# Optimization experiments

Hardware: AMD Instinct MI355X
Metric: run time of the kernel (lower is better)

The kernel has to match this reference:

```python
import jax, jax.numpy as jnp
import numpy as np

BETA = 0.95      # LIF membrane decay (init arg)
THR = 1.0        # snntorch Leaky default threshold
NUM_STEPS = 128


@jax.custom_vjp
def spike(x):
    # Heaviside fire with ATan surrogate gradient (snntorch default, alpha=2)
    return (x > 0).astype(x.dtype)

def _spike_fwd(x):
    return spike(x), x

def _spike_bwd(x, g):
    return (g / (1.0 + (jnp.pi * x) ** 2),)

spike.defvjp(_spike_fwd, _spike_bwd)


def setup_inputs() -> dict:
    key = jax.random.key(0)
    ks = jax.random.split(key, 5)
    B, NI, NH, NO = 2048, 1024, 2048, 10
    return {
        "x": jax.random.normal(ks[0], (B, NI), dtype=jnp.float32),
        "w1": jax.random.normal(ks[1], (NH, NI), dtype=jnp.float32) * 0.05,
        "b1": jax.random.normal(ks[2], (NH,), dtype=jnp.float32) * 0.05,
        "w2": jax.random.normal(ks[3], (NO, NH), dtype=jnp.float32) * 0.05,
        "b2": jax.random.normal(ks[4], (NO,), dtype=jnp.float32) * 0.05,
    }


def reference(x, w1, b1, w2, b2):
    # fc1(x) is loop-invariant: compute the input current once.
    cur1 = jnp.einsum("bi,hi->bh", x, w1) + b1  # [B, NH]
    mem1_0 = jnp.zeros_like(cur1)
    mem2_0 = jnp.zeros((x.shape[0], w2.shape[0]), dtype=x.dtype)

    def step(carry, _):
        mem1, mem2 = carry
        # snntorch Leaky, reset-by-subtraction; reset term is detached.
        reset1 = jax.lax.stop_gradient((mem1 > THR).astype(mem1.dtype))
        mem1 = BETA * mem1 + cur1 - reset1 * THR
        spk1 = spike(mem1 - THR)
        cur2 = jnp.einsum("bh,oh->bo", spk1, w2) + b2  # [B, NO]
        reset2 = jax.lax.stop_gradient((mem2 > THR).astype(mem2.dtype))
        mem2 = BETA * mem2 + cur2 - reset2 * THR
        spk2 = spike(mem2 - THR)
        return (mem1, mem2), (spk2, mem2)

    _, (spk2_rec, mem2_rec) = jax.lax.scan(step, (mem1_0, mem2_0), None, length=NUM_STEPS)
    return spk2_rec, mem2_rec  # each [T, B, NO]
```

## Files before the change

kernel.cpp:

```cpp
#include <hip/hip_runtime.h>
#include <hip/hip_bf16.h>


#define B_   2048
#define NI_  1024
#define NH_  2048
#define NO_  10
#define T_   128

typedef __attribute__((ext_vector_type(8))) short short8;
typedef __attribute__((ext_vector_type(4))) float f32x4;
typedef __attribute__((ext_vector_type(4))) unsigned int u32x4;

__device__ __forceinline__ unsigned int bf16_rne(float f) {
  unsigned int u = __float_as_uint(f);
  return (u + 0x7FFFu + ((u >> 16) & 1u)) >> 16;
}

#define G_ASTRIDE 144
#define G_AOFF    0
#define G_BOFF    (128 * G_ASTRIDE)
#define G_SMEM    (2 * 128 * G_ASTRIDE)

__global__ __launch_bounds__(512, 2) void gemm_cur1(
    const float* __restrict__ x, const float* __restrict__ w1,
    const float* __restrict__ b1, float* __restrict__ cur1) {
  __shared__ __align__(16) char smem[G_SMEM];
  const int tid = threadIdx.x;
  const int lane = tid & 63;
  const int wv = tid >> 6;
  const int wm = wv >> 2;
  const int wn = wv & 3;
  const int n15 = lane & 15;
  const int g = lane >> 4;
  const int brow = blockIdx.y * 128;
  const int bcol = blockIdx.x * 128;
  const int r_st = tid >> 3;
  const int kq = tid & 7;

  f32x4 acc[4][2];
#pragma unroll
  for (int tm = 0; tm < 4; ++tm)
#pragma unroll
    for (int tn = 0; tn < 2; ++tn) acc[tm][tn] = f32x4{0, 0, 0, 0};

  for (int kt = 0; kt < NI_; kt += 32) {
#pragma unroll
    for (int p = 0; p < 2; ++p) {
      const int r = r_st + p * 64;
      const float4 va = *reinterpret_cast<const float4*>(
          &x[(size_t)(brow + r) * NI_ + kt + kq * 4]);
      const float4 vb = *reinterpret_cast<const float4*>(
          &w1[(size_t)(bcol + r) * NI_ + kt + kq * 4]);
      const float fa[4] = {va.x, va.y, va.z, va.w};
      const float fb[4] = {vb.x, vb.y, vb.z, vb.w};
      unsigned ha[4], la[4], hb[4], lb[4];
#pragma unroll
      for (int c = 0; c < 4; ++c) {
        ha[c] = bf16_rne(fa[c]);
        la[c] = bf16_rne(fa[c] - __uint_as_float(ha[c] << 16));
        hb[c] = bf16_rne(fb[c]);
        lb[c] = bf16_rne(fb[c] - __uint_as_float(hb[c] << 16));
      }
      char* arow = smem + G_AOFF + r * G_ASTRIDE;
      char* brw  = smem + G_BOFF + r * G_ASTRIDE;
      *reinterpret_cast<uint2*>(arow + kq * 8) =
          uint2{ha[0] | (ha[1] << 16), ha[2] | (ha[3] << 16)};
      *reinterpret_cast<uint2*>(arow + 64 + kq * 8) =
          uint2{la[0] | (la[1] << 16), la[2] | (la[3] << 16)};
      *reinterpret_cast<uint2*>(brw + kq * 8) =
          uint2{hb[0] | (hb[1] << 16), hb[2] | (hb[3] << 16)};
      *reinterpret_cast<uint2*>(brw + 64 + kq * 8) =
          uint2{lb[0] | (lb[1] << 16), lb[2] | (lb[3] << 16)};
    }
    __syncthreads();

    short8 bh2[2], bl2[2];
#pragma unroll
    for (int tn = 0; tn < 2; ++tn) {
      const char* p = smem + G_BOFF + (wn * 32 + tn * 16 + n15) * G_ASTRIDE;
      bh2[tn] = *reinterpret_cast<const short8*>(p + g * 16);
      bl2[tn] = *reinterpret_cast<const short8*>(p + 64 + g * 16);
    }
#pragma unroll
    for (int tm = 0; tm < 4; ++tm) {
      const char* p = smem + G_AOFF + (wm * 64 + tm * 16 + n15) * G_ASTRIDE;
      const short8 ah = *reinterpret_cast<const short8*>(p + g * 16);
      const short8 al = *reinterpret_cast<const short8*>(p + 64 + g * 16);
#pragma unroll
      for (int tn = 0; tn < 2; ++tn) {
        acc[tm][tn] = __builtin_amdgcn_mfma_f32_16x16x32_bf16(
            ah, bh2[tn], acc[tm][tn], 0, 0, 0);
        acc[tm][tn] = __builtin_amdgcn_mfma_f32_16x16x32_bf16(
            ah, bl2[tn], acc[tm][tn], 0, 0, 0);
        acc[tm][tn] = __builtin_amdgcn_mfma_f32_16x16x32_bf16(
            al, bh2[tn], acc[tm][tn], 0, 0, 0);
      }
    }
    __syncthreads();
  }

#pragma unroll
  for (int tn = 0; tn < 2; ++tn) {
    const int col = bcol + wn * 32 + tn * 16 + n15;
    const float bias = b1[col];
#pragma unroll
    for (int tm = 0; tm < 4; ++tm) {
      const int rowb = brow + wm * 64 + tm * 16 + g * 4;
#pragma unroll
      for (int r = 0; r < 4; ++r)
        cur1[(size_t)(rowb + r) * NH_ + col] = acc[tm][tn][r] + bias;
    }
  }
}

__global__ __launch_bounds__(512, 4) void spikegen(
    const float* __restrict__ cur1, unsigned char* __restrict__ bits8) {
  const int lane = threadIdx.x & 63;
  const int w = threadIdx.x >> 6;
  const int bq = w >> 2;
  const int qf = w & 3;
  const int bb = blockIdx.x * 2 + bq;

  float mem1[8], c1v[8], c1m[8], cc[8];
  {
    const float* base = cur1 + (size_t)bb * NH_ + qf * 512 + lane * 8;
#pragma unroll
    for (int q = 0; q < 2; ++q) {
      const float4 v = *reinterpret_cast<const float4*>(base + q * 4);
      c1v[q * 4 + 0] = v.x; c1v[q * 4 + 1] = v.y;
      c1v[q * 4 + 2] = v.z; c1v[q * 4 + 3] = v.w;
    }
#pragma unroll
    for (int i = 0; i < 8; ++i) {
      mem1[i] = 0.0f;
      c1m[i] = c1v[i] - 1.0f;
      cc[i] = c1v[i];
    }
  }

  const float vone = 1.0f;
  unsigned char* dst = bits8 + (size_t)bb * T_ * 256 + qf * 64 + lane;
  for (int t = 0; t < T_; ++t) {
    float Wf = 0.0f;
#pragma unroll
    for (int i = 7; i >= 0; --i) {
      const float m = fmaf(0.95f, mem1[i], cc[i]);
      mem1[i] = m;
      const bool c = m > 1.0f;
      const float s = c ? vone : 0.0f;
      Wf = fmaf(2.0f, Wf, s);
      cc[i] = c ? c1m[i] : c1v[i];
    }
    dst[t * 256] = (unsigned char)(unsigned)Wf;
  }
}

#define SO_TC 16

__global__ __launch_bounds__(512, 2) void snn_out(
    const unsigned* __restrict__ bitsg, const float* __restrict__ w2,
    const float* __restrict__ b2, float* __restrict__ spk2_rec,
    float* __restrict__ mem2_rec) {
  __shared__ uint2 lut[16];
  __shared__ __align__(16) unsigned bitsl[64 * 68];
  __shared__ __align__(16) float comb[8 * 640];
  const int tid = threadIdx.x;
  const int lane = tid & 63;
  const int w = tid >> 6;
  const int bbase = blockIdx.x * 4;

  if (tid < 16) {
    lut[tid] = uint2{(tid & 1 ? 0x3F80u : 0u) | (tid & 2 ? 0x3F800000u : 0u),
                     (tid & 4 ? 0x3F80u : 0u) | (tid & 8 ? 0x3F800000u : 0u)};
  }

  u32x4 bhi[8];
  {
    const int o = lane & 15;
    const int koff = (lane >> 4) * 8;
#pragma unroll
    for (int kbl = 0; kbl < 8; ++kbl) {
      const int kb = w * 8 + kbl;
      unsigned int hw[4];
#pragma unroll
      for (int p = 0; p < 4; ++p) {
        unsigned int h0 = 0, h1 = 0;
        if (o < NO_) {
          const int k = kb * 32 + koff + p * 2;
          h0 = bf16_rne(w2[(size_t)o * NH_ + k]);
          h1 = bf16_rne(w2[(size_t)o * NH_ + k + 1]);
        }
        hw[p] = h0 | (h1 << 16);
      }
      bhi[kbl] = u32x4{hw[0], hw[1], hw[2], hw[3]};
    }
  }

  float mem2 = 0.0f, spk2 = 0.0f, b2v = 0.0f;
  float *srec = nullptr, *mrec = nullptr;
  if (w < 4 && lane < NO_) {
    b2v = b2[lane];
    srec = spk2_rec + (size_t)(bbase + w) * NO_ + lane;
    mrec = mem2_rec + (size_t)(bbase + w) * NO_ + lane;
  }

  const int n15 = lane & 15;
  const int g = lane >> 4;
  const unsigned char* bytes = reinterpret_cast<const unsigned char*>(bitsl);

  for (int ch = 0; ch < T_ / SO_TC; ++ch) {
#pragma unroll
    for (int j = 0; j < 2; ++j) {
      const int q = tid + j * 512;
      const int row = q >> 4;
      const int kq = q & 15;
      const int b = row >> 4, tl = row & 15;
      const uint4 v = *reinterpret_cast<const uint4*>(
          bitsg + ((size_t)(bbase + b) * T_ + ch * SO_TC + tl) * 64 + kq * 4);
      *reinterpret_cast<uint4*>(bitsl + row * 68 + kq * 4) = v;
    }
    __syncthreads();

#pragma unroll
    for (int b = 0; b < 4; ++b) {
      const int rbase = ((b * SO_TC + n15) * 68 + w * 8) * 4 + g;
      f32x4 acc = {0.0f, 0.0f, 0.0f, 0.0f};
#pragma unroll
      for (int kbl = 0; kbl < 8; ++kbl) {
        const unsigned byt = bytes[rbase + kbl * 4];
        const uint2 lo2 = lut[byt & 15u];
        const uint2 hi2 = lut[byt >> 4];
        const u32x4 A = {lo2.x, lo2.y, hi2.x, hi2.y};
        const short8 af = __builtin_bit_cast(short8, A);
        acc = __builtin_amdgcn_mfma_f32_16x16x32_bf16(
            af, __builtin_bit_cast(short8, bhi[kbl]), acc, 0, 0, 0);
      }
      if (n15 < NO_)
        *reinterpret_cast<f32x4*>(
            &comb[w * 640 + b * 160 + g * 40 + n15 * 4]) = acc;
    }
    __syncthreads();

    if (w < 4 && lane < NO_) {
      const float* cbase = comb + w * 160 + lane * 4;
#pragma unroll
      for (int tl = 0; tl < SO_TC; ++tl) {
        const int off = (tl >> 2) * 40 + (tl & 3);
        float s = 0.0f;
#pragma unroll
        for (int kk = 0; kk < 8; ++kk) s += cbase[kk * 640 + off];
        const float cur2 = s + b2v;
        float m = fmaf(0.95f, mem2, cur2);
        m = m - spk2;
        mem2 = m;
        spk2 = (m > 1.0f) ? 1.0f : 0.0f;
        const int t = ch * SO_TC + tl;
        srec[(size_t)t * (B_ * NO_)] = spk2;
        mrec[(size_t)t * (B_ * NO_)] = m;
      }
    }
  }
}

#define CUR1_BYTES ((size_t)B_ * NH_ * 4)
#define BITS_BYTES ((size_t)B_ * T_ * 64 * 4)

extern "C" void kernel_launch(void* const* d_in, const int* in_sizes, int n_in,
                              void* d_out, int out_size, void* d_ws, size_t ws_size,
                              hipStream_t stream) {
  const float* x  = (const float*)d_in[0];
  const float* w1 = (const float*)d_in[1];
  const float* b1 = (const float*)d_in[2];
  const float* w2 = (const float*)d_in[3];
  const float* b2 = (const float*)d_in[4];
  float* out = (float*)d_out;
  float* cur1 = (float*)d_ws;
  unsigned* bitsg = (unsigned*)((char*)d_ws + CUR1_BYTES);

  float* spk2_rec = out;
  float* mem2_rec = out + (size_t)T_ * B_ * NO_;

  dim3 g1(NH_ / 128, B_ / 128);
  gemm_cur1<<<g1, 512, 0, stream>>>(x, w1, b1, cur1);
  spikegen<<<B_ / 2, 512, 0, stream>>>(cur1, (unsigned char*)bitsg);
  snn_out<<<B_ / 4, 512, 0, stream>>>(bitsg, w2, b2, spk2_rec, mem2_rec);
}
```

Before: 170.8 us.

## Precompute split-bf16 operands in a separate pass and run GEMM over concatenated K

Adds a conversion kernel that splits x and w1 into bf16 hi/lo parts once and lays them out as a 3072-wide K dimension (hi,hi,lo for x and hi,lo,hi for w1), so the three-product split-precision GEMM becomes a plain bf16 GEMM. The GEMM no longer repeats the float-to-bf16 conversion inside every tile, which removes redundant conversion work, and its tile shrinks to 64x128 so more blocks are launched. The cost is an extra kernel launch plus writing and re-reading roughly 37 MB of converted operands. The converted buffers sit in workspace memory that the spike-bits buffer also uses, which is safe only because the GEMM finishes before spikegen writes there.

```diff
diff --git a/kernel.cpp b/kernel.cpp
--- a/kernel.cpp
+++ b/kernel.cpp
@@ -7,6 +7,7 @@
 #define NH_  2048
 #define NO_  10
 #define T_   128
+#define KP   3072
 
 typedef __attribute__((ext_vector_type(8))) short short8;
 typedef __attribute__((ext_vector_type(4))) float f32x4;
@@ -17,15 +18,45 @@
   return (u + 0x7FFFu + ((u >> 16) & 1u)) >> 16;
 }
 
-#define G_ASTRIDE 144
-#define G_AOFF    0
-#define G_BOFF    (128 * G_ASTRIDE)
-#define G_SMEM    (2 * 128 * G_ASTRIDE)
+__global__ __launch_bounds__(256) void convert_hl(
+    const float* __restrict__ x, const float* __restrict__ w1,
+    unsigned short* __restrict__ xc, unsigned short* __restrict__ w1c) {
+  const int gidx = blockIdx.x * 256 + threadIdx.x;
+  const int mat = gidx >> 19;
+  const int loc = gidx & 524287;
+  const int row = loc >> 8;
+  const int kq = loc & 255;
+
+  const float* src = (mat ? w1 : x) + (size_t)row * NI_ + kq * 4;
+  unsigned short* dst = (mat ? w1c : xc) + (size_t)row * KP + kq * 4;
+  const int hi2_off = mat ? 2048 : 1024;
+  const int lo_off  = mat ? 1024 : 2048;
+
+  const float4 v = *reinterpret_cast<const float4*>(src);
+  const float f[4] = {v.x, v.y, v.z, v.w};
+  unsigned h[4], l[4];
+#pragma unroll
+  for (int c = 0; c < 4; ++c) {
+    h[c] = bf16_rne(f[c]);
+    l[c] = bf16_rne(f[c] - __uint_as_float(h[c] << 16));
+  }
+  const uint2 hw = uint2{h[0] | (h[1] << 16), h[2] | (h[3] << 16)};
+  const uint2 lw = uint2{l[0] | (l[1] << 16), l[2] | (l[3] << 16)};
+  *reinterpret_cast<uint2*>(dst) = hw;
+  *reinterpret_cast<uint2*>(dst + hi2_off) = hw;
+  *reinterpret_cast<uint2*>(dst + lo_off) = lw;
+}
+
+#define RS 144
+#define GA_OFF 0
+#define GB_OFF (64 * RS)
+#define G2_SMEM (GB_OFF + 128 * RS)
 
 __global__ __launch_bounds__(512, 2) void gemm_cur1(
-    const float* __restrict__ x, const float* __restrict__ w1,
+    const unsigned short* __restrict__ xc,
+    const unsigned short* __restrict__ w1c,
     const float* __restrict__ b1, float* __restrict__ cur1) {
-  __shared__ __align__(16) char smem[G_SMEM];
+  __shared__ __align__(16) char smem[G2_SMEM];
   const int tid = threadIdx.x;
   const int lane = tid & 63;
   const int wv = tid >> 6;
@@ -33,69 +64,51 @@
   const int wn = wv & 3;
   const int n15 = lane & 15;
   const int g = lane >> 4;
-  const int brow = blockIdx.y * 128;
+  const int brow = blockIdx.y * 64;
   const int bcol = blockIdx.x * 128;
-  const int r_st = tid >> 3;
-  const int kq = tid & 7;
-
-  f32x4 acc[4][2];
-#pragma unroll
-  for (int tm = 0; tm < 4; ++tm)
+
+  const int s_row = tid >> 3;
+  const int s_o16 = tid & 7;
+
+  f32x4 acc[2][2];
+#pragma unroll
+  for (int tm = 0; tm < 2; ++tm)
 #pragma unroll
     for (int tn = 0; tn < 2; ++tn) acc[tm][tn] = f32x4{0, 0, 0, 0};
 
-  for (int kt = 0; kt < NI_; kt += 32) {
+  for (int kt = 0; kt < KP; kt += 64) {
+    {
+      const uint4 v = *reinterpret_cast<const uint4*>(
+          xc + (size_t)(brow + s_row) * KP + kt + s_o16 * 8);
+      *reinterpret_cast<uint4*>(smem + GA_OFF + s_row * RS + s_o16 * 16) = v;
+    }
 #pragma unroll
     for (int p = 0; p < 2; ++p) {
-      const int r = r_st + p * 64;
-      const float4 va = *reinterpret_cast<const float4*>(
-          &x[(size_t)(brow + r) * NI_ + kt + kq * 4]);
-      const float4 vb = *reinterpret_cast<const float4*>(
-          &w1[(size_t)(bcol + r) * NI_ + kt + kq * 4]);
-      const float fa[4] = {va.x, va.y, va.z, va.w};
-      const float fb[4] = {vb.x, vb.y, vb.z, vb.w};
-      unsigned ha[4], la[4], hb[4], lb[4];
-#pragma unroll
-      for (int c = 0; c < 4; ++c) {
-        ha[c] = bf16_rne(fa[c]);
-        la[c] = bf16_rne(fa[c] - __uint_as_float(ha[c] << 16));
-        hb[c] = bf16_rne(fb[c]);
-        lb[c] = bf16_rne(fb[c] - __uint_as_float(hb[c] << 16));
-      }
-      char* arow = smem + G_AOFF + r * G_ASTRIDE;
-      char* brw  = smem + G_BOFF + r * G_ASTRIDE;
-      *reinterpret_cast<uint2*>(arow + kq * 8) =
-          uint2{ha[0] | (ha[1] << 16), ha[2] | (ha[3] << 16)};
-      *reinterpret_cast<uint2*>(arow + 64 + kq * 8) =
-          uint2{la[0] | (la[1] << 16), la[2] | (la[3] << 16)};
-      *reinterpret_cast<uint2*>(brw + kq * 8) =
-          uint2{hb[0] | (hb[1] << 16), hb[2] | (hb[3] << 16)};
-      *reinterpret_cast<uint2*>(brw + 64 + kq * 8) =
-          uint2{lb[0] | (lb[1] << 16), lb[2] | (lb[3] << 16)};
+      const int s = tid + p * 512;
+      const int row = s >> 3, o16 = s & 7;
+      const uint4 v = *reinterpret_cast<const uint4*>(
+          w1c + (size_t)(bcol + row) * KP + kt + o16 * 8);
+      *reinterpret_cast<uint4*>(smem + GB_OFF + row * RS + o16 * 16) = v;
     }
     __syncthreads();
 
-    short8 bh2[2], bl2[2];
-#pragma unroll
-    for (int tn = 0; tn < 2; ++tn) {
-      const char* p = smem + G_BOFF + (wn * 32 + tn * 16 + n15) * G_ASTRIDE;
-      bh2[tn] = *reinterpret_cast<const short8*>(p + g * 16);
-      bl2[tn] = *reinterpret_cast<const short8*>(p + 64 + g * 16);
-    }
-#pragma unroll
-    for (int tm = 0; tm < 4; ++tm) {
-      const char* p = smem + G_AOFF + (wm * 64 + tm * 16 + n15) * G_ASTRIDE;
-      const short8 ah = *reinterpret_cast<const short8*>(p + g * 16);
-      const short8 al = *reinterpret_cast<const short8*>(p + 64 + g * 16);
-#pragma unroll
-      for (int tn = 0; tn < 2; ++tn) {
-        acc[tm][tn] = __builtin_amdgcn_mfma_f32_16x16x32_bf16(
-            ah, bh2[tn], acc[tm][tn], 0, 0, 0);
-        acc[tm][tn] = __builtin_amdgcn_mfma_f32_16x16x32_bf16(
-            ah, bl2[tn], acc[tm][tn], 0, 0, 0);
-        acc[tm][tn] = __builtin_amdgcn_mfma_f32_16x16x32_bf16(
-            al, bh2[tn], acc[tm][tn], 0, 0, 0);
-      }
+#pragma unroll
+    for (int kk = 0; kk < 2; ++kk) {
+      short8 af[2], bf[2];
+#pragma unroll
+      for (int tm = 0; tm < 2; ++tm)
+        af[tm] = *reinterpret_cast<const short8*>(
+            smem + GA_OFF + (wm * 32 + tm * 16 + n15) * RS + kk * 64 + g * 16);
+#pragma unroll
+      for (int tn = 0; tn < 2; ++tn)
+        bf[tn] = *reinterpret_cast<const short8*>(
+            smem + GB_OFF + (wn * 32 + tn * 16 + n15) * RS + kk * 64 + g * 16);
+#pragma unroll
+      for (int tm = 0; tm < 2; ++tm)
+#pragma unroll
+        for (int tn = 0; tn < 2; ++tn)
+          acc[tm][tn] = __builtin_amdgcn_mfma_f32_16x16x32_bf16(
+              af[tm], bf[tn], acc[tm][tn], 0, 0, 0);
     }
     __syncthreads();
   }
@@ -105,8 +118,8 @@
     const int col = bcol + wn * 32 + tn * 16 + n15;
     const float bias = b1[col];
 #pragma unroll
-    for (int tm = 0; tm < 4; ++tm) {
-      const int rowb = brow + wm * 64 + tm * 16 + g * 4;
+    for (int tm = 0; tm < 2; ++tm) {
+      const int rowb = brow + wm * 32 + tm * 16 + g * 4;
 #pragma unroll
       for (int r = 0; r < 4; ++r)
         cur1[(size_t)(rowb + r) * NH_ + col] = acc[tm][tn][r] + bias;
@@ -264,7 +277,6 @@
 }
 
 #define CUR1_BYTES ((size_t)B_ * NH_ * 4)
-#define BITS_BYTES ((size_t)B_ * T_ * 64 * 4)
 
 extern "C" void kernel_launch(void* const* d_in, const int* in_sizes, int n_in,
                               void* d_out, int out_size, void* d_ws, size_t ws_size,
@@ -276,13 +288,16 @@
   const float* b2 = (const float*)d_in[4];
   float* out = (float*)d_out;
   float* cur1 = (float*)d_ws;
+  unsigned short* xc  = (unsigned short*)((char*)d_ws + CUR1_BYTES);
+  unsigned short* w1c = xc + (size_t)2048 * KP;
   unsigned* bitsg = (unsigned*)((char*)d_ws + CUR1_BYTES);
 
   float* spk2_rec = out;
   float* mem2_rec = out + (size_t)T_ * B_ * NO_;
 
-  dim3 g1(NH_ / 128, B_ / 128);
-  gemm_cur1<<<g1, 512, 0, stream>>>(x, w1, b1, cur1);
+  convert_hl<<<4096, 256, 0, stream>>>(x, w1, xc, w1c);
+  dim3 g1(NH_ / 128, B_ / 64);
+  gemm_cur1<<<g1, 512, 0, stream>>>(xc, w1c, b1, cur1);
   spikegen<<<B_ / 2, 512, 0, stream>>>(cur1, (unsigned char*)bitsg);
   snn_out<<<B_ / 4, 512, 0, stream>>>(bitsg, w2, b2, spk2_rec, mem2_rec);
 }
```

After: 172.3 us. Within noise of the previous version (+0.9%).
